# Optimization experiments

Measured on AMD Instinct MI355X. Metric: run time of the kernel, lower is better.

Reference implementation:

```python
import jax, jax.numpy as jnp
import numpy as np

D_MODEL = 1024
NUM_HEADS = 16
HEAD_DIM = D_MODEL // NUM_HEADS
B, L = 4, 2048


def setup_inputs() -> dict:
    key = jax.random.key(0)
    ks = jax.random.split(key, 10)
    s = 1.0 / np.sqrt(D_MODEL)
    inp = {
        "x": jax.random.normal(ks[0], (B, L, D_MODEL), dtype=jnp.float32),
        "mask": jax.random.randint(ks[1], (1, 1, L, L), 0, 2, dtype=jnp.int32),
        "Wq": jax.random.normal(ks[2], (D_MODEL, D_MODEL), dtype=jnp.float32) * s,
        "bq": jnp.zeros((D_MODEL,), dtype=jnp.float32),
        "Wk": jax.random.normal(ks[3], (D_MODEL, D_MODEL), dtype=jnp.float32) * s,
        "bk": jnp.zeros((D_MODEL,), dtype=jnp.float32),
        "Wv": jax.random.normal(ks[4], (D_MODEL, D_MODEL), dtype=jnp.float32) * s,
        "bv": jnp.zeros((D_MODEL,), dtype=jnp.float32),
        "Wo": jax.random.normal(ks[5], (D_MODEL, D_MODEL), dtype=jnp.float32) * s,
        "bo": jnp.zeros((D_MODEL,), dtype=jnp.float32),
    }
    return inp


def reference(x, mask, Wq, bq, Wk, bk, Wv, bv, Wo, bo):
    b, l, d = x.shape
    # projections (torch Linear: x @ W.T + b)
    q = (x @ Wq.T + bq).reshape(b, l, NUM_HEADS, HEAD_DIM).transpose(0, 2, 1, 3)
    k = (x @ Wk.T + bk).reshape(b, l, NUM_HEADS, HEAD_DIM).transpose(0, 2, 1, 3)
    v = (x @ Wv.T + bv).reshape(b, l, NUM_HEADS, HEAD_DIM).transpose(0, 2, 1, 3)
    scale = 1.0 / np.sqrt(HEAD_DIM).astype(np.float32)
    scores = jnp.einsum("bhqd,bhkd->bhqk", q, k) * scale
    scores = jnp.where(mask == 0, jnp.float32(-1e9), scores)
    attn = jax.nn.softmax(scores, axis=-1)
    out = jnp.einsum("bhqk,bhkd->bhqd", attn, v)
    out = out.transpose(0, 2, 1, 3).reshape(b, l, d)
    return out @ Wo.T + bo
```

## Files before the change

### kernel.cpp

```cpp
#include <hip/hip_runtime.h>
#include <stdint.h>

#define LSEQ 2048
#define DMODEL 1024
#define NHEADS 16
#define HDIM 64
#define NBATCH 4

typedef __attribute__((ext_vector_type(8))) __bf16 bf16x8;
typedef __attribute__((ext_vector_type(4))) __bf16 bf16x4;
typedef __attribute__((ext_vector_type(4))) float f32x4;
typedef __attribute__((ext_vector_type(16))) float f32x16;
typedef __attribute__((ext_vector_type(4))) uint32_t u32x4;
typedef __attribute__((ext_vector_type(8))) uint16_t u16x8;
typedef __attribute__((ext_vector_type(4))) uint16_t u16x4;

__device__ inline float fexp2(float x) {
#if __has_builtin(__builtin_amdgcn_exp2f)
    return __builtin_amdgcn_exp2f(x);
#else
    float r; asm("v_exp_f32 %0, %1" : "=v"(r) : "v"(x)); return r;
#endif
}

__device__ inline uint32_t bitmask1(uint32_t m, int pos) {
#if __has_builtin(__builtin_amdgcn_sbfe)
    return (uint32_t)__builtin_amdgcn_sbfe((int)m, pos, 1);
#else
    return (uint32_t)(((int32_t)(m << (31 - pos))) >> 31);
#endif
}

__device__ inline uint32_t cvtpk(float lo, float hi) {
    uint32_t r;
    asm("v_cvt_pk_bf16_f32 %0, %1, %2" : "=v"(r) : "v"(lo), "v"(hi));
    return r;
}
__device__ inline void swap32(uint32_t& a, uint32_t& b) {
    asm volatile("v_permlane32_swap_b32 %0, %1" : "+v"(a), "+v"(b));
}

__device__ inline void gload_lds16(const void* g, const void* l) {
    auto gp = reinterpret_cast<const uint32_t __attribute__((address_space(1)))*>(
        reinterpret_cast<uintptr_t>(g));
    auto lp = reinterpret_cast<uint32_t __attribute__((address_space(3)))*>(
        (uint32_t)(uintptr_t)(l));
    __builtin_amdgcn_global_load_lds(gp, lp, 16, 0, 0);
}

__device__ inline f32x16 zero16() {
    f32x16 z;
#pragma unroll
    for (int i = 0; i < 16; i++) z[i] = 0.f;
    return z;
}

__global__ void cvt_f32_bf16(const float* __restrict__ src, __bf16* __restrict__ dst, int n) {
    int idx = blockIdx.x * blockDim.x + threadIdx.x;
    int stride = gridDim.x * blockDim.x;
    for (int i = idx * 4; i < n; i += stride * 4) {
        float4 f = *(const float4*)(src + i);
        bf16x4 v;
        v[0] = (__bf16)f.x; v[1] = (__bf16)f.y; v[2] = (__bf16)f.z; v[3] = (__bf16)f.w;
        *(bf16x4*)(dst + i) = v;
    }
}

__global__ void cvt_w4(const float* __restrict__ a, const float* __restrict__ b,
                       const float* __restrict__ c, const float* __restrict__ d,
                       __bf16* __restrict__ dst,
                       const float* __restrict__ bq, const float* __restrict__ bk,
                       const float* __restrict__ bv, float* __restrict__ bqkv) {
    const int t = blockIdx.x * blockDim.x + threadIdx.x;
    const int i4 = t * 4;
    const int m = i4 >> 20;
    const int off = i4 & ((1 << 20) - 1);
    const float* src = (m == 0) ? a : (m == 1) ? b : (m == 2) ? c : d;
    float4 f = *(const float4*)(src + off);
    bf16x4 v;
    v[0] = (__bf16)f.x; v[1] = (__bf16)f.y; v[2] = (__bf16)f.z; v[3] = (__bf16)f.w;
    *(bf16x4*)(dst + i4) = v;
    if (blockIdx.x < 12) {
        const int i = blockIdx.x * 256 + threadIdx.x;
        bqkv[i] = (i < 1024) ? bq[i] : (i < 2048) ? bk[i - 1024] : bv[i - 2048];
    }
}

__global__ void pack_mask(const int* __restrict__ mask, unsigned long long* __restrict__ mbits) {
    const int row = blockIdx.x;
    const int w = threadIdx.x >> 6, lane = threadIdx.x & 63;
    const int* mrow = mask + (size_t)row * LSEQ;
#pragma unroll
    for (int it = 0; it < 8; it++) {
        const int c = it * 256 + w * 64 + lane;
        const unsigned long long b = __ballot(mrow[c] != 0);
        if (lane == 0) mbits[(size_t)row * 32 + it * 4 + w] = b;
    }
}

template <int MODE>
__global__ __launch_bounds__(256) void gemm_bt(const __bf16* __restrict__ A,
                                               const __bf16* __restrict__ Bw,
                                               const float* __restrict__ bias,
                                               void* __restrict__ Cout,
                                               int M, int N, int K, float scale) {
    __shared__ __bf16 As[128 * 32];
    __shared__ __bf16 Bs[128 * 32];

    const int nwg = gridDim.x;
    int bid = blockIdx.x;
    bid = (bid & 7) * (nwg >> 3) + (bid >> 3);

    const int nbn = N >> 7;
    const int bm = (bid / nbn) << 7;
    const int bn = (bid % nbn) << 7;
    const int tid = threadIdx.x;
    const int w = tid >> 6, lane = tid & 63;
    const int l15 = lane & 15, l4 = lane >> 4;
    const int wm = (w >> 1) * 64, wn = (w & 1) * 64;

    f32x4 acc[4][4];
    for (int i = 0; i < 4; i++)
        for (int j = 0; j < 4; j++)
            acc[i][j] = (f32x4){0.f, 0.f, 0.f, 0.f};

    const int fa0 = (w * 2 + 0) * 64 + lane;
    const int fa1 = (w * 2 + 1) * 64 + lane;
    const __bf16* gA0 = A + (size_t)(bm + (fa0 >> 2)) * K + (fa0 & 3) * 8;
    const __bf16* gA1 = A + (size_t)(bm + (fa1 >> 2)) * K + (fa1 & 3) * 8;
    const __bf16* gB0 = Bw + (size_t)(bn + (fa0 >> 2)) * K + (fa0 & 3) * 8;
    const __bf16* gB1 = Bw + (size_t)(bn + (fa1 >> 2)) * K + (fa1 & 3) * 8;
    const __bf16* lA0 = &As[(w * 2 + 0) * 512];
    const __bf16* lA1 = &As[(w * 2 + 1) * 512];
    const __bf16* lB0 = &Bs[(w * 2 + 0) * 512];
    const __bf16* lB1 = &Bs[(w * 2 + 1) * 512];

    for (int kt = 0; kt < K; kt += 32) {
        __syncthreads();
        gload_lds16(gA0 + kt, lA0);
        gload_lds16(gA1 + kt, lA1);
        gload_lds16(gB0 + kt, lB0);
        gload_lds16(gB1 + kt, lB1);
        __syncthreads();

        bf16x8 af[4], bw[4];
        for (int i = 0; i < 4; i++)
            af[i] = *(const bf16x8*)&As[(wm + i * 16 + l15) * 32 + l4 * 8];
        for (int j = 0; j < 4; j++)
            bw[j] = *(const bf16x8*)&Bs[(wn + j * 16 + l15) * 32 + l4 * 8];
        for (int i = 0; i < 4; i++)
            for (int j = 0; j < 4; j++)
                acc[i][j] = __builtin_amdgcn_mfma_f32_16x16x32_bf16(af[i], bw[j], acc[i][j], 0, 0, 0);
    }

    for (int i = 0; i < 4; i++) {
        const int row0 = bm + wm + i * 16 + l4 * 4;
        for (int j = 0; j < 4; j++) {
            const int col = bn + wn + j * 16 + l15;
            const float bv = bias[col];
            if (MODE == 0) {
                __bf16* dst = (__bf16*)Cout;
                const int which = col >> 10;
                const int cr = col & 1023;
                const int h = cr >> 6, d = cr & 63;
                const float scl = (which == 0) ? scale : 1.0f;
                for (int jj = 0; jj < 4; jj++) {
                    const int r = row0 + jj;
                    const int b = r >> 11, l = r & (LSEQ - 1);
                    dst[((size_t)which << 23) +
                        (((size_t)(b * NHEADS + h) * LSEQ + l) << 6) + d] =
                        (__bf16)((acc[i][j][jj] + bv) * scl);
                }
            } else {
                float* dst = (float*)Cout;
                for (int jj = 0; jj < 4; jj++) {
                    const int r = row0 + jj;
                    dst[(size_t)r * N + col] = acc[i][j][jj] + bv;
                }
            }
        }
    }
}

__device__ inline void storeV4(uint32_t (*vt)[32], int kpi, int d0,
                               const u16x4& r0, const u16x4& r1) {
    const uint32_t* a = (const uint32_t*)&r0;
    const uint32_t* b = (const uint32_t*)&r1;
#pragma unroll
    for (int jp = 0; jp < 2; jp++) {
        const uint32_t w0 = __builtin_amdgcn_perm(b[jp], a[jp], 0x05040100u);
        const uint32_t w1 = __builtin_amdgcn_perm(b[jp], a[jp], 0x07060302u);
        const int da = d0 + jp * 2, db = da + 1;
        vt[da][(kpi & 3) | (((kpi >> 2) ^ (da & 7)) << 2)] = w0;
        vt[db][(kpi & 3) | (((kpi >> 2) ^ (db & 7)) << 2)] = w1;
    }
}

__global__ __launch_bounds__(512) void attn_fwd(const __bf16* __restrict__ Q,
                                                const __bf16* __restrict__ Kk,
                                                const __bf16* __restrict__ V,
                                                const unsigned long long* __restrict__ mbits,
                                                __bf16* __restrict__ Oout) {
    const int bh = blockIdx.x & 63;
    const int qt = blockIdx.x >> 6;
    const int tid = threadIdx.x;
    const int w = tid >> 6, lane = tid & 63;
    const int l31 = lane & 31, hi = lane >> 5, l7 = lane & 7;

    __shared__ __bf16 Ks[2][64 * 64];
    __shared__ uint32_t Vt32[2][64][32];

    const int q0w = qt * 256 + w * 32;

    const __bf16* qrow = Q + ((size_t)bh * LSEQ + q0w + l31) * HDIM + hi * 8;
    bf16x8 aq[4];
#pragma unroll
    for (int s = 0; s < 4; s++) aq[s] = *(const bf16x8*)(qrow + s * 16);

    const u32x4 onesu = {0x3F803F80u, 0x3F803F80u, 0x3F803F80u, 0x3F803F80u};
    const bf16x8 ones = __builtin_bit_cast(bf16x8, onesu);

    f32x16 o0 = zero16(), o1 = zero16(), lacc = zero16();

    const int ck = tid;
    const int koff = ((ck >> 3) << 7) + ((((ck & 7) ^ ((ck >> 3) & 7))) << 4);
    const char* kp0 = (const char*)(Kk + (size_t)bh * LSEQ * HDIM) + koff;
    const int kdst = ck * 8;

    const int kpi = tid & 31;
    const int d0v = (tid >> 5) * 4;
    const __bf16* vp0 = V + (size_t)bh * LSEQ * HDIM + (size_t)(2 * kpi) * HDIM + d0v;
    const __bf16* vp1 = vp0 + HDIM;

    const uint2* mptr = (const uint2*)(mbits + (size_t)(q0w + l31) * 32);
    const int msh = hi * 4;

    {
        const u16x4 v0 = *(const u16x4*)(vp0);
        const u16x4 v1 = *(const u16x4*)(vp1);
        vp0 += 64 * HDIM; vp1 += 64 * HDIM;
        storeV4(Vt32[0], kpi, d0v, v0, v1);
        gload_lds16(kp0, &Ks[0][kdst]);
        kp0 += 8192;
    }
    __syncthreads();

    int cur = 0;
    const int NT = LSEQ / 64;
    for (int t = 0; t < NT; t++) {
        const int nx = cur ^ 1;
        u16x4 nv0, nv1;
        if (t < NT - 1) {
            nv0 = *(const u16x4*)(vp0);
            nv1 = *(const u16x4*)(vp1);
            vp0 += 64 * HDIM; vp1 += 64 * HDIM;
            gload_lds16(kp0, &Ks[nx][kdst]);
            kp0 += 8192;
        }

        const uint2 mw = mptr[t];
        const uint32_t mword0 = mw.x >> msh;
        const uint32_t mword1 = mw.y >> msh;
        const char* ksb = (const char*)&Ks[cur][0];
        const uint32_t* vb = &Vt32[cur][0][0];

#pragma unroll
        for (int kk = 0; kk < 2; kk++) {
            f32x16 sf = zero16();
            __builtin_amdgcn_s_setprio(1);
#pragma unroll
            for (int s = 0; s < 4; s++) {
                const bf16x8 ka = *(const bf16x8*)(ksb + kk * 4096 + l31 * 128 +
                                                   (((s * 2 + hi) ^ l7) << 4));
                sf = __builtin_amdgcn_mfma_f32_32x32x16_bf16(ka, aq[s], sf, 0, 0, 0);
            }
            __builtin_amdgcn_s_setprio(0);

            const uint32_t mwd = kk ? mword1 : mword0;
            float e[16];
#pragma unroll
            for (int r = 0; r < 16; r++) {
                float ev = fexp2(sf[r]);
                const uint32_t msk = bitmask1(mwd, (r & 3) + 8 * (r >> 2));
                e[r] = __builtin_bit_cast(float, __builtin_bit_cast(uint32_t, ev) & msk);
            }
            uint32_t p0 = cvtpk(e[0], e[1]),   p1 = cvtpk(e[2], e[3]);
            uint32_t p2 = cvtpk(e[4], e[5]),   p3 = cvtpk(e[6], e[7]);
            uint32_t p4 = cvtpk(e[8], e[9]),   p5 = cvtpk(e[10], e[11]);
            uint32_t p6 = cvtpk(e[12], e[13]), p7 = cvtpk(e[14], e[15]);
            swap32(p0, p2); swap32(p1, p3);
            swap32(p4, p6); swap32(p5, p7);
            const bf16x8 pa0 = __builtin_bit_cast(bf16x8, (u32x4){p0, p1, p2, p3});
            const bf16x8 pa1 = __builtin_bit_cast(bf16x8, (u32x4){p4, p5, p6, p7});

            __builtin_amdgcn_s_setprio(1);
            lacc = __builtin_amdgcn_mfma_f32_32x32x16_bf16(pa0, ones, lacc, 0, 0, 0);
            lacc = __builtin_amdgcn_mfma_f32_32x32x16_bf16(pa1, ones, lacc, 0, 0, 0);
#pragma unroll
            for (int s2 = 0; s2 < 2; s2++) {
                const bf16x8 pa = s2 ? pa1 : pa0;
                const int col = (((kk * 4 + s2 * 2 + hi) ^ l7) << 2);
                const u32x4 v0 = *(const u32x4*)(vb + (l31) * 32 + col);
                const u32x4 v1 = *(const u32x4*)(vb + (32 + l31) * 32 + col);
                o0 = __builtin_amdgcn_mfma_f32_32x32x16_bf16(pa, __builtin_bit_cast(bf16x8, v0), o0, 0, 0, 0);
                o1 = __builtin_amdgcn_mfma_f32_32x32x16_bf16(pa, __builtin_bit_cast(bf16x8, v1), o1, 0, 0, 0);
            }
            __builtin_amdgcn_s_setprio(0);
        }

        if (t < NT - 1) storeV4(Vt32[nx], kpi, d0v, nv0, nv1);
        __syncthreads();
        cur = nx;
    }

    const int b = bh >> 4, h = bh & 15;
#pragma unroll
    for (int r = 0; r < 16; r++) {
        const float invr = 1.0f / fmaxf(lacc[r], 1e-30f);
        const int q = q0w + (r & 3) + 8 * (r >> 2) + 4 * hi;
        const size_t base = ((size_t)b * LSEQ + q) * DMODEL + h * HDIM + l31;
        Oout[base] = (__bf16)(o0[r] * invr);
        Oout[base + 32] = (__bf16)(o1[r] * invr);
    }
}

extern "C" void kernel_launch(void* const* d_in, const int* in_sizes, int n_in,
                              void* d_out, int out_size, void* d_ws, size_t ws_size,
                              hipStream_t stream) {
    const float* x  = (const float*)d_in[0];
    const int* mask = (const int*)d_in[1];
    const float* Wq = (const float*)d_in[2];
    const float* bq = (const float*)d_in[3];
    const float* Wk = (const float*)d_in[4];
    const float* bk = (const float*)d_in[5];
    const float* Wv = (const float*)d_in[6];
    const float* bv = (const float*)d_in[7];
    const float* Wo = (const float*)d_in[8];
    const float* bo = (const float*)d_in[9];

    char* ws = (char*)d_ws;
    __bf16* xb  = (__bf16*)(ws);
    __bf16* wqb = (__bf16*)(ws + (16u << 20));
    __bf16* wob = (__bf16*)(ws + (22u << 20));
    __bf16* qb  = (__bf16*)(ws + (24u << 20));
    __bf16* ab  = (__bf16*)(ws + (72u << 20));
    unsigned long long* mb = (unsigned long long*)(ws + (88u << 20));
    float* bqkv = (float*)(ws + (89u << 20));

    const __bf16* kb = qb + ((size_t)1 << 23);
    const __bf16* vb = qb + ((size_t)2 << 23);

    const int M = NBATCH * LSEQ;
    const int N = DMODEL;
    const int K = DMODEL;
    const float cs = 0.18033688011112f;

    cvt_f32_bf16<<<2048, 256, 0, stream>>>(x, xb, M * K);
    cvt_w4<<<4096, 256, 0, stream>>>(Wq, Wk, Wv, Wo, wqb, bq, bk, bv, bqkv);
    pack_mask<<<LSEQ, 256, 0, stream>>>(mask, mb);

    gemm_bt<0><<<(M / 128) * (3 * N / 128), 256, 0, stream>>>(
        xb, wqb, bqkv, (void*)qb, M, 3 * N, K, cs);

    attn_fwd<<<(LSEQ / 256) * 64, 512, 0, stream>>>(qb, kb, vb, mb, ab);

    gemm_bt<1><<<(M / 128) * (N / 128), 256, 0, stream>>>(
        ab, wob, bo, d_out, M, N, K, 1.0f);
}
```

Before: 220.3 us.

## Double attention key tile to 128 and fold mask into score accumulator init

Each loop iteration of the attention kernel now processes 128 keys instead of 64. K and V are staged with two async LDS loads and wider 16-byte V loads, which halves the number of block barriers and loop overheads. Masking moves from an AND applied after exp2 to an initial accumulator value of -300 for masked positions, so the MFMA output already carries the mask bias. That removes per-element masking work after the exponent. In exchange, LDS use doubles to 64KB per block, which can reduce the number of resident blocks per CU.

```diff
diff --git a/kernel.cpp b/kernel.cpp
--- a/kernel.cpp
+++ b/kernel.cpp
@@ -13,7 +13,6 @@
 typedef __attribute__((ext_vector_type(16))) float f32x16;
 typedef __attribute__((ext_vector_type(4))) uint32_t u32x4;
 typedef __attribute__((ext_vector_type(8))) uint16_t u16x8;
-typedef __attribute__((ext_vector_type(4))) uint16_t u16x4;
 
 __device__ inline float fexp2(float x) {
 #if __has_builtin(__builtin_amdgcn_exp2f)
@@ -46,13 +45,6 @@
     auto lp = reinterpret_cast<uint32_t __attribute__((address_space(3)))*>(
         (uint32_t)(uintptr_t)(l));
     __builtin_amdgcn_global_load_lds(gp, lp, 16, 0, 0);
-}
-
-__device__ inline f32x16 zero16() {
-    f32x16 z;
-#pragma unroll
-    for (int i = 0; i < 16; i++) z[i] = 0.f;
-    return z;
 }
 
 __global__ void cvt_f32_bf16(const float* __restrict__ src, __bf16* __restrict__ dst, int n) {
@@ -182,17 +174,17 @@
     }
 }
 
-__device__ inline void storeV4(uint32_t (*vt)[32], int kpi, int d0,
-                               const u16x4& r0, const u16x4& r1) {
+__device__ inline void storeV8w(uint32_t (*vt)[64], int kpi, int d0,
+                                const u16x8& r0, const u16x8& r1) {
     const uint32_t* a = (const uint32_t*)&r0;
     const uint32_t* b = (const uint32_t*)&r1;
 #pragma unroll
-    for (int jp = 0; jp < 2; jp++) {
+    for (int jp = 0; jp < 4; jp++) {
         const uint32_t w0 = __builtin_amdgcn_perm(b[jp], a[jp], 0x05040100u);
         const uint32_t w1 = __builtin_amdgcn_perm(b[jp], a[jp], 0x07060302u);
         const int da = d0 + jp * 2, db = da + 1;
-        vt[da][(kpi & 3) | (((kpi >> 2) ^ (da & 7)) << 2)] = w0;
-        vt[db][(kpi & 3) | (((kpi >> 2) ^ (db & 7)) << 2)] = w1;
+        vt[da][(kpi & 3) | ((((kpi >> 2) ^ (da & 7))) << 2)] = w0;
+        vt[db][(kpi & 3) | ((((kpi >> 2) ^ (db & 7))) << 2)] = w1;
     }
 }
 
@@ -207,8 +199,8 @@
     const int w = tid >> 6, lane = tid & 63;
     const int l31 = lane & 31, hi = lane >> 5, l7 = lane & 7;
 
-    __shared__ __bf16 Ks[2][64 * 64];
-    __shared__ uint32_t Vt32[2][64][32];
+    __shared__ __bf16 Ks[2][128 * 64];
+    __shared__ uint32_t Vt32[2][64][64];
 
     const int q0w = qt * 256 + w * 32;
 
@@ -220,53 +212,66 @@
     const u32x4 onesu = {0x3F803F80u, 0x3F803F80u, 0x3F803F80u, 0x3F803F80u};
     const bf16x8 ones = __builtin_bit_cast(bf16x8, onesu);
 
-    f32x16 o0 = zero16(), o1 = zero16(), lacc = zero16();
-
-    const int ck = tid;
-    const int koff = ((ck >> 3) << 7) + ((((ck & 7) ^ ((ck >> 3) & 7))) << 4);
-    const char* kp0 = (const char*)(Kk + (size_t)bh * LSEQ * HDIM) + koff;
-    const int kdst = ck * 8;
-
-    const int kpi = tid & 31;
-    const int d0v = (tid >> 5) * 4;
+    f32x16 o0, o1, lacc;
+#pragma unroll
+    for (int i = 0; i < 16; i++) { o0[i] = 0.f; o1[i] = 0.f; lacc[i] = 0.f; }
+
+    const int ck0 = tid, ck1 = tid + 512;
+    const int koff0 = ((ck0 >> 3) << 7) + ((((ck0 & 7) ^ ((ck0 >> 3) & 7))) << 4);
+    const int koff1 = ((ck1 >> 3) << 7) + ((((ck1 & 7) ^ ((ck1 >> 3) & 7))) << 4);
+    const char* kp0 = (const char*)(Kk + (size_t)bh * LSEQ * HDIM) + koff0;
+    const char* kp1 = (const char*)(Kk + (size_t)bh * LSEQ * HDIM) + koff1;
+    const int kdst0 = ck0 * 8, kdst1 = ck1 * 8;
+
+    const int kpi = tid & 63;
+    const int d0v = (tid >> 6) * 8;
     const __bf16* vp0 = V + (size_t)bh * LSEQ * HDIM + (size_t)(2 * kpi) * HDIM + d0v;
     const __bf16* vp1 = vp0 + HDIM;
 
-    const uint2* mptr = (const uint2*)(mbits + (size_t)(q0w + l31) * 32);
+    const uint4* mptr = (const uint4*)(mbits + (size_t)(q0w + l31) * 32);
     const int msh = hi * 4;
 
     {
-        const u16x4 v0 = *(const u16x4*)(vp0);
-        const u16x4 v1 = *(const u16x4*)(vp1);
-        vp0 += 64 * HDIM; vp1 += 64 * HDIM;
-        storeV4(Vt32[0], kpi, d0v, v0, v1);
-        gload_lds16(kp0, &Ks[0][kdst]);
-        kp0 += 8192;
+        const u16x8 v0 = *(const u16x8*)(vp0);
+        const u16x8 v1 = *(const u16x8*)(vp1);
+        vp0 += 128 * HDIM; vp1 += 128 * HDIM;
+        storeV8w(Vt32[0], kpi, d0v, v0, v1);
+        gload_lds16(kp0, &Ks[0][kdst0]);
+        gload_lds16(kp1, &Ks[0][kdst1]);
+        kp0 += 16384; kp1 += 16384;
     }
     __syncthreads();
 
     int cur = 0;
-    const int NT = LSEQ / 64;
+    const int NT = LSEQ / 128;
     for (int t = 0; t < NT; t++) {
         const int nx = cur ^ 1;
-        u16x4 nv0, nv1;
+        u16x8 nv0, nv1;
         if (t < NT - 1) {
-            nv0 = *(const u16x4*)(vp0);
-            nv1 = *(const u16x4*)(vp1);
-            vp0 += 64 * HDIM; vp1 += 64 * HDIM;
-            gload_lds16(kp0, &Ks[nx][kdst]);
-            kp0 += 8192;
+            nv0 = *(const u16x8*)(vp0);
+            nv1 = *(const u16x8*)(vp1);
+            vp0 += 128 * HDIM; vp1 += 128 * HDIM;
+            gload_lds16(kp0, &Ks[nx][kdst0]);
+            gload_lds16(kp1, &Ks[nx][kdst1]);
+            kp0 += 16384; kp1 += 16384;
         }
 
-        const uint2 mw = mptr[t];
-        const uint32_t mword0 = mw.x >> msh;
-        const uint32_t mword1 = mw.y >> msh;
+        const uint4 mw = mptr[t];
         const char* ksb = (const char*)&Ks[cur][0];
         const uint32_t* vb = &Vt32[cur][0][0];
 
 #pragma unroll
-        for (int kk = 0; kk < 2; kk++) {
-            f32x16 sf = zero16();
+        for (int kk = 0; kk < 4; kk++) {
+            const uint32_t mwd = (kk == 0) ? mw.x : (kk == 1) ? mw.y
+                               : (kk == 2) ? mw.z : mw.w;
+            const uint32_t inv = ~(mwd >> msh);
+            f32x16 sf;
+#pragma unroll
+            for (int r = 0; r < 16; r++) {
+                const uint32_t neg = bitmask1(inv, (r & 3) + 8 * (r >> 2)) & 0xC3960000u;
+                sf[r] = __builtin_bit_cast(float, neg);
+            }
+
             __builtin_amdgcn_s_setprio(1);
 #pragma unroll
             for (int s = 0; s < 4; s++) {
@@ -276,14 +281,9 @@
             }
             __builtin_amdgcn_s_setprio(0);
 
-            const uint32_t mwd = kk ? mword1 : mword0;
             float e[16];
 #pragma unroll
-            for (int r = 0; r < 16; r++) {
-                float ev = fexp2(sf[r]);
-                const uint32_t msk = bitmask1(mwd, (r & 3) + 8 * (r >> 2));
-                e[r] = __builtin_bit_cast(float, __builtin_bit_cast(uint32_t, ev) & msk);
-            }
+            for (int r = 0; r < 16; r++) e[r] = fexp2(sf[r]);
             uint32_t p0 = cvtpk(e[0], e[1]),   p1 = cvtpk(e[2], e[3]);
             uint32_t p2 = cvtpk(e[4], e[5]),   p3 = cvtpk(e[6], e[7]);
             uint32_t p4 = cvtpk(e[8], e[9]),   p5 = cvtpk(e[10], e[11]);
@@ -300,15 +300,15 @@
             for (int s2 = 0; s2 < 2; s2++) {
                 const bf16x8 pa = s2 ? pa1 : pa0;
                 const int col = (((kk * 4 + s2 * 2 + hi) ^ l7) << 2);
-                const u32x4 v0 = *(const u32x4*)(vb + (l31) * 32 + col);
-                const u32x4 v1 = *(const u32x4*)(vb + (32 + l31) * 32 + col);
+                const u32x4 v0 = *(const u32x4*)(vb + l31 * 64 + col);
+                const u32x4 v1 = *(const u32x4*)(vb + (32 + l31) * 64 + col);
                 o0 = __builtin_amdgcn_mfma_f32_32x32x16_bf16(pa, __builtin_bit_cast(bf16x8, v0), o0, 0, 0, 0);
                 o1 = __builtin_amdgcn_mfma_f32_32x32x16_bf16(pa, __builtin_bit_cast(bf16x8, v1), o1, 0, 0, 0);
             }
             __builtin_amdgcn_s_setprio(0);
         }
 
-        if (t < NT - 1) storeV4(Vt32[nx], kpi, d0v, nv0, nv1);
+        if (t < NT - 1) storeV8w(Vt32[nx], kpi, d0v, nv0, nv1);
         __syncthreads();
         cur = nx;
     }
```

New measurement: 234.4 us. +6.4%, slower.
